# Kernel optimization log

Hardware: AMD Instinct MI355X
Metric: run time of the kernel (lower is better)

## Reference

```python
import jax, jax.numpy as jnp
import numpy as np

N_EMBD = 1024
N_HEAD = 16
HEAD_DIM = N_EMBD // N_HEAD
HIDDEN = int(2 * N_EMBD * 4 / 3)  # 2730, SwiGLU sizing from source
EPS = 1e-5


def setup_inputs() -> dict:
    key = jax.random.key(0)
    ks = jax.random.split(key, 16)
    def lin(k, fan_in, fan_out):
        bound = 1.0 / np.sqrt(fan_in)
        return jax.random.uniform(k, (fan_in, fan_out), jnp.float32, -bound, bound)
    return {
        "x": jax.random.normal(ks[0], (2, 2048, N_EMBD), jnp.float32),
        "ln1_g": jnp.ones((N_EMBD,), jnp.float32),
        "ln1_b": jnp.zeros((N_EMBD,), jnp.float32),
        "qkv_w": lin(ks[1], N_EMBD, 3 * N_EMBD),
        "qkv_b": jnp.zeros((3 * N_EMBD,), jnp.float32),
        "proj_w": lin(ks[2], N_EMBD, N_EMBD),
        "proj_b": jnp.zeros((N_EMBD,), jnp.float32),
        "ln2_g": jnp.ones((N_EMBD,), jnp.float32),
        "ln2_b": jnp.zeros((N_EMBD,), jnp.float32),
        "gate_w": lin(ks[3], N_EMBD, HIDDEN),
        "gate_b": jnp.zeros((HIDDEN,), jnp.float32),
        "up_w": lin(ks[4], N_EMBD, HIDDEN),
        "up_b": jnp.zeros((HIDDEN,), jnp.float32),
        "down_w": lin(ks[5], HIDDEN, N_EMBD),
        "down_b": jnp.zeros((N_EMBD,), jnp.float32),
    }


def _layernorm(x, g, b):
    mu = jnp.mean(x, axis=-1, keepdims=True)
    var = jnp.mean(jnp.square(x - mu), axis=-1, keepdims=True)
    return (x - mu) * jax.lax.rsqrt(var + EPS) * g + b


def _alibi_slopes(n_heads):
    i = jnp.arange(1, n_heads + 1, dtype=jnp.float32)
    return 1.0 / jnp.power(2.0, 8.0 * i / n_heads)  # [H]


def reference(x, ln1_g, ln1_b, qkv_w, qkv_b, proj_w, proj_b,
              ln2_g, ln2_b, gate_w, gate_b, up_w, up_b, down_w, down_b):
    B, T, C = x.shape
    residual = x
    h = _layernorm(x, ln1_g, ln1_b)
    qkv = h @ qkv_w + qkv_b  # [B,T,3C]
    q, k, v = jnp.split(qkv, 3, axis=-1)
    q = q.reshape(B, T, N_HEAD, HEAD_DIM).transpose(0, 2, 1, 3)
    k = k.reshape(B, T, N_HEAD, HEAD_DIM).transpose(0, 2, 1, 3)
    v = v.reshape(B, T, N_HEAD, HEAD_DIM).transpose(0, 2, 1, 3)
    scale = 1.0 / np.sqrt(HEAD_DIM)
    attn = jnp.einsum('bhqd,bhkd->bhqk', q, k) * scale
    # ALiBi: slope * |q_pos - k_pos| (abs distance, as in source)
    pos = jnp.arange(T)
    dist = jnp.abs(pos[None, :] - pos[:, None]).astype(jnp.float32)  # [T,T]
    slopes = _alibi_slopes(N_HEAD)  # [H]
    attn = attn + slopes[None, :, None, None] * dist[None, None, :, :]
    causal = pos[:, None] >= pos[None, :]  # tril mask
    attn = jnp.where(causal[None, None], attn, -jnp.inf)
    attn = jax.nn.softmax(attn, axis=-1)
    out = jnp.einsum('bhqk,bhkd->bhqd', attn, v)
    out = out.transpose(0, 2, 1, 3).reshape(B, T, C)
    out = out @ proj_w + proj_b
    x = residual + out
    residual = x
    h = _layernorm(x, ln2_g, ln2_b)
    gate = h @ gate_w + gate_b
    up = h @ up_w + up_b
    ff = (gate * jax.nn.sigmoid(gate) * up) @ down_w + down_b
    return residual + ff
```

## Files before the change

### kernel.cpp

```cpp
#include <hip/hip_runtime.h>
#include <cstdint>
#include <cstddef>

#define T_SEQ   2048
#define BATCH   2
#define NEMBD   1024
#define NHEAD   16
#define HDIM    64
#define HIDDEN  2730
#define HIDDENP 2816
#define MROWS   4096

typedef __bf16 bf16x8 __attribute__((ext_vector_type(8)));
typedef __bf16 bf16x4 __attribute__((ext_vector_type(4)));
typedef float  f32x4  __attribute__((ext_vector_type(4)));

__device__ __forceinline__ void gl2lds16(const void* g, void* l) {
    __builtin_amdgcn_global_load_lds((const __attribute__((address_space(1))) void*)g,
                                     (__attribute__((address_space(3))) void*)l, 16, 0, 0);
}

__global__ __launch_bounds__(256) void conv_trans(const float* __restrict__ W,
                                                  __bf16* __restrict__ Wt,
                                                  int K, int N, int Kp)
{
    __shared__ float tile[32][33];
    const int n0 = blockIdx.x * 32, k0 = blockIdx.y * 32;
    const int tx = threadIdx.x, ty = threadIdx.y;
#pragma unroll
    for (int i = ty; i < 32; i += 8) {
        int k = k0 + i, n = n0 + tx;
        tile[i][tx] = (k < K && n < N) ? W[(size_t)k * N + n] : 0.f;
    }
    __syncthreads();
#pragma unroll
    for (int i = ty; i < 32; i += 8) {
        int n = n0 + i, k = k0 + tx;
        Wt[(size_t)n * Kp + k] = (__bf16)tile[tx][i];
    }
}

__global__ __launch_bounds__(256) void ln_kernel(const float* __restrict__ x,
                                                 const float* __restrict__ g,
                                                 const float* __restrict__ b,
                                                 __bf16* __restrict__ out)
{
    const int row = blockIdx.x;
    const int t   = threadIdx.x;
    const float4 v = ((const float4*)(x + (size_t)row * NEMBD))[t];
    float s  = v.x + v.y + v.z + v.w;
    float sq = v.x * v.x + v.y * v.y + v.z * v.z + v.w * v.w;
#pragma unroll
    for (int d = 1; d < 64; d <<= 1) { s += __shfl_xor(s, d); sq += __shfl_xor(sq, d); }
    __shared__ float ssh[4], sqsh[4];
    const int w = t >> 6;
    if ((t & 63) == 0) { ssh[w] = s; sqsh[w] = sq; }
    __syncthreads();
    s  = ssh[0] + ssh[1] + ssh[2] + ssh[3];
    sq = sqsh[0] + sqsh[1] + sqsh[2] + sqsh[3];
    const float mean = s * (1.f / NEMBD);
    const float var  = sq * (1.f / NEMBD) - mean * mean;
    const float rstd = rsqrtf(var + 1e-5f);
    const float4 gg = ((const float4*)g)[t];
    const float4 bb = ((const float4*)b)[t];
    bf16x4 o;
    o[0] = (__bf16)((v.x - mean) * rstd * gg.x + bb.x);
    o[1] = (__bf16)((v.y - mean) * rstd * gg.y + bb.y);
    o[2] = (__bf16)((v.z - mean) * rstd * gg.z + bb.z);
    o[3] = (__bf16)((v.w - mean) * rstd * gg.w + bb.w);
    *(bf16x4*)&out[(size_t)row * NEMBD + t * 4] = o;
}

template <int MODE>
__global__ __launch_bounds__(256) void gemm_bt(const __bf16* __restrict__ A,
                                               const __bf16* __restrict__ Bt,
                                               const float* __restrict__ bias, int Nreal,
                                               const float* __restrict__ res,
                                               const __bf16* __restrict__ gbuf,
                                               void* __restrict__ outp,
                                               void* __restrict__ outp2,
                                               int Kp, int N)
{
    __shared__ alignas(16) __bf16 Ash[128 * 32];
    __shared__ alignas(16) __bf16 Bsh[128 * 32];
    const int tid  = threadIdx.x;
    const int w    = tid >> 6, l = tid & 63;
    const int ln   = l & 15, quad = l >> 4;
    const int wm   = w >> 1, wn = w & 1;
    const long m0  = (long)blockIdx.y * 128;
    const long n0  = (long)blockIdx.x * 128;
    f32x4 acc[4][4] = {};
    const __bf16* Ab = A + m0 * Kp;
    const __bf16* Bb = Bt + n0 * Kp;
    const int arow = l >> 2, acol = (l & 3) * 8;

    for (int k0 = 0; k0 < Kp; k0 += 32) {
#pragma unroll
        for (int it = 0; it < 2; ++it) {
            const int c = w * 2 + it;
            gl2lds16(Ab + (long)(c * 16 + arow) * Kp + k0 + acol, Ash + c * 512);
            gl2lds16(Bb + (long)(c * 16 + arow) * Kp + k0 + acol, Bsh + c * 512);
        }
        __syncthreads();
        bf16x8 af[4], bfr[4];
#pragma unroll
        for (int i = 0; i < 4; ++i) {
            af[i]  = *(const bf16x8*)&Ash[(wm * 64 + i * 16 + ln) * 32 + quad * 8];
            bfr[i] = *(const bf16x8*)&Bsh[(wn * 64 + i * 16 + ln) * 32 + quad * 8];
        }
#pragma unroll
        for (int tm = 0; tm < 4; ++tm)
#pragma unroll
            for (int tn = 0; tn < 4; ++tn)
                acc[tm][tn] = __builtin_amdgcn_mfma_f32_16x16x32_bf16(af[tm], bfr[tn], acc[tm][tn], 0, 0, 0);
        __syncthreads();
    }

    if (MODE == 3 && n0 >= 2048) {
        __bf16* vt = (__bf16*)outp2;
        const long bbq    = m0 >> 11;
        const long t0base = (m0 & 2047) + wm * 64;
#pragma unroll
        for (int tm = 0; tm < 4; ++tm)
#pragma unroll
            for (int tn = 0; tn < 4; ++tn) {
                const long col = n0 + wn * 64 + tn * 16 + ln;
                const float bv = bias[col];
                bf16x4 pv;
#pragma unroll
                for (int r = 0; r < 4; ++r) pv[r] = (__bf16)(acc[tm][tn][r] + bv);
                const long tt = t0base + tm * 16 + quad * 4;
                *(bf16x4*)&vt[(bbq * 1024 + (col - 2048)) * 2048 + tt] = pv;
            }
        return;
    }

#pragma unroll
    for (int tm = 0; tm < 4; ++tm)
#pragma unroll
        for (int tn = 0; tn < 4; ++tn) {
            const long col = n0 + wn * 64 + tn * 16 + ln;
            const float bv = (col < Nreal) ? bias[col] : 0.f;
#pragma unroll
            for (int r = 0; r < 4; ++r) {
                const long row = m0 + wm * 64 + tm * 16 + quad * 4 + r;
                float v = acc[tm][tn][r] + bv;
                if (MODE == 0) {
                    ((__bf16*)outp)[row * N + col] = (__bf16)v;
                } else if (MODE == 1) {
                    ((float*)outp)[row * N + col] = v + res[row * N + col];
                } else if (MODE == 2) {
                    const float gg = (float)gbuf[row * N + col];
                    const float sg = gg / (1.f + __expf(-gg));
                    ((__bf16*)outp)[row * N + col] = (__bf16)(sg * v);
                } else {
                    ((__bf16*)outp)[row * 2048 + col] = (__bf16)v;
                }
            }
        }
}

__global__ __launch_bounds__(256) void attn_kernel(const __bf16* __restrict__ qk,
                                                   const __bf16* __restrict__ vT,
                                                   __bf16* __restrict__ out)
{
    __shared__ alignas(16) __bf16 Ksh[64 * 64];
    __shared__ alignas(16) __bf16 Vtsh[64 * 64];
    __shared__ alignas(16) __bf16 Psh[4][32 * 64];

    const int tid = threadIdx.x;
    const int w   = tid >> 6, l = tid & 63;
    const int ln  = l & 15, quad = l >> 4;
    const int bh  = blockIdx.x;
    const int qt  = 15 - blockIdx.y;
    const int bb  = bh >> 4, hh = bh & 15;
    const long bT = (long)bb * T_SEQ;
    const int q0b = qt * 128;
    const int q0w = q0b + w * 32;
    const float slope = exp2f(-0.5f * (float)(hh + 1));

    bf16x8 qf[2][2];
#pragma unroll
    for (int q2 = 0; q2 < 2; ++q2) {
        const __bf16* qp = qk + (bT + q0w + q2 * 16 + ln) * 2048 + hh * 64 + quad * 8;
        qf[q2][0] = *(const bf16x8*)qp;
        qf[q2][1] = *(const bf16x8*)(qp + 32);
    }

    f32x4 o[2][4] = {};
    float mrun[2][4], lrun[2][4];
#pragma unroll
    for (int q2 = 0; q2 < 2; ++q2)
#pragma unroll
        for (int r = 0; r < 4; ++r) { mrun[q2][r] = -1e30f; lrun[q2][r] = 0.f; }

    const int sw = ln & 7;
    const int kmax = q0b + 128;
    for (int k0 = 0; k0 < kmax; k0 += 64) {
        __syncthreads();
#pragma unroll
        for (int jj = 0; jj < 2; ++jj) {
            const int j   = w * 2 + jj;
            const int row = j * 8 + (l >> 3);
            const int seg = (l & 7) ^ (row & 7);
            gl2lds16(qk + (bT + k0 + row) * 2048 + 1024 + hh * 64 + seg * 8,
                     Ksh + j * 8 * 64);
            gl2lds16(vT + ((long)(bb * 1024 + hh * 64 + row)) * 2048 + k0 + seg * 8,
                     Vtsh + j * 8 * 64);
        }
        __syncthreads();

        if (k0 <= q0w + 31) {
            const bool act0 = (k0 <= q0w + 15);
            f32x4 s0[4], s1[4];
#pragma unroll
            for (int kt = 0; kt < 4; ++kt) { s0[kt] = (f32x4){0,0,0,0}; s1[kt] = (f32x4){0,0,0,0}; }
#pragma unroll
            for (int kt = 0; kt < 4; ++kt)
#pragma unroll
                for (int kh = 0; kh < 2; ++kh) {
                    const bf16x8 kf = *(const bf16x8*)&Ksh[(kt * 16 + ln) * 64 + (((kh * 4 + quad) ^ sw) << 3)];
                    if (act0) s0[kt] = __builtin_amdgcn_mfma_f32_16x16x32_bf16(qf[0][kh], kf, s0[kt], 0, 0, 0);
                    s1[kt] = __builtin_amdgcn_mfma_f32_16x16x32_bf16(qf[1][kh], kf, s1[kt], 0, 0, 0);
                }
            float alpha[2][4];
#pragma unroll
            for (int q2 = 0; q2 < 2; ++q2) {
                if (q2 == 0 && !act0) continue;
                f32x4* s = (q2 == 0) ? s0 : s1;
                const int qbase = q0w + q2 * 16;
                float rmax[4];
#pragma unroll
                for (int r = 0; r < 4; ++r) {
                    const int qrow = qbase + quad * 4 + r;
                    float mv = -1e30f;
#pragma unroll
                    for (int kt = 0; kt < 4; ++kt) {
                        const int kc = k0 + kt * 16 + ln;
                        float v = s[kt][r] * 0.125f + slope * (float)(qrow - kc);
                        v = (kc <= qrow) ? v : -1e30f;
                        s[kt][r] = v;
                        mv = fmaxf(mv, v);
                    }
                    rmax[r] = mv;
                }
#pragma unroll
                for (int d = 1; d < 16; d <<= 1)
#pragma unroll
                    for (int r = 0; r < 4; ++r) rmax[r] = fmaxf(rmax[r], __shfl_xor(rmax[r], d));
                float rsum[4];
#pragma unroll
                for (int r = 0; r < 4; ++r) {
                    const float mnew = fmaxf(mrun[q2][r], rmax[r]);
                    alpha[q2][r] = __expf(mrun[q2][r] - mnew);
                    mrun[q2][r]  = mnew;
                    float t = 0.f;
#pragma unroll
                    for (int kt = 0; kt < 4; ++kt) {
                        const float e = __expf(s[kt][r] - mnew);
                        s[kt][r] = e;
                        t += e;
                    }
                    rsum[r] = t;
                }
#pragma unroll
                for (int d = 1; d < 16; d <<= 1)
#pragma unroll
                    for (int r = 0; r < 4; ++r) rsum[r] += __shfl_xor(rsum[r], d);
#pragma unroll
                for (int r = 0; r < 4; ++r) lrun[q2][r] = lrun[q2][r] * alpha[q2][r] + rsum[r];
#pragma unroll
                for (int kt = 0; kt < 4; ++kt)
#pragma unroll
                    for (int r = 0; r < 4; ++r) {
                        const int q = q2 * 16 + quad * 4 + r;
                        Psh[w][q * 64 + (((kt * 2 + (ln >> 3)) ^ (q & 7)) << 3) + (ln & 7)] = (__bf16)s[kt][r];
                    }
#pragma unroll
                for (int dt = 0; dt < 4; ++dt)
#pragma unroll
                    for (int r = 0; r < 4; ++r) o[q2][dt][r] *= alpha[q2][r];
            }
            asm volatile("s_waitcnt lgkmcnt(0)" ::: "memory");
#pragma unroll
            for (int kh2 = 0; kh2 < 2; ++kh2) {
                bf16x8 pf0, pf1;
                if (act0) pf0 = *(const bf16x8*)&Psh[w][(ln)*64 + (((kh2 * 4 + quad) ^ sw) << 3)];
                pf1 = *(const bf16x8*)&Psh[w][(16 + ln) * 64 + (((kh2 * 4 + quad) ^ sw) << 3)];
#pragma unroll
                for (int dt = 0; dt < 4; ++dt) {
                    const bf16x8 vf = *(const bf16x8*)&Vtsh[(dt * 16 + ln) * 64 + (((kh2 * 4 + quad) ^ sw) << 3)];
                    if (act0) o[0][dt] = __builtin_amdgcn_mfma_f32_16x16x32_bf16(pf0, vf, o[0][dt], 0, 0, 0);
                    o[1][dt] = __builtin_amdgcn_mfma_f32_16x16x32_bf16(pf1, vf, o[1][dt], 0, 0, 0);
                }
            }
        }
    }
#pragma unroll
    for (int q2 = 0; q2 < 2; ++q2)
#pragma unroll
        for (int dt = 0; dt < 4; ++dt)
#pragma unroll
            for (int r = 0; r < 4; ++r) {
                const long row = bT + q0w + q2 * 16 + quad * 4 + r;
                out[row * NEMBD + hh * 64 + dt * 16 + ln] = (__bf16)(o[q2][dt][r] / lrun[q2][r]);
            }
}

extern "C" void kernel_launch(void* const* d_in, const int* in_sizes, int n_in,
                              void* d_out, int out_size, void* d_ws, size_t ws_size,
                              hipStream_t stream)
{
    const float* x      = (const float*)d_in[0];
    const float* ln1_g  = (const float*)d_in[1];
    const float* ln1_b  = (const float*)d_in[2];
    const float* qkv_w  = (const float*)d_in[3];
    const float* qkv_b  = (const float*)d_in[4];
    const float* proj_w = (const float*)d_in[5];
    const float* proj_b = (const float*)d_in[6];
    const float* ln2_g  = (const float*)d_in[7];
    const float* ln2_b  = (const float*)d_in[8];
    const float* gate_w = (const float*)d_in[9];
    const float* gate_b = (const float*)d_in[10];
    const float* up_w   = (const float*)d_in[11];
    const float* up_b   = (const float*)d_in[12];
    const float* down_w = (const float*)d_in[13];
    const float* down_b = (const float*)d_in[14];
    float* out = (float*)d_out;
    char*  ws  = (char*)d_ws;

    const size_t OFF_WQKV  = 0;
    const size_t OFF_WPROJ = 6291456;
    const size_t OFF_WGATE = 8388608;
    const size_t OFF_WUP   = 14155776;
    const size_t OFF_WDOWN = 19922944;
    const size_t OFF_H     = 25690112;
    const size_t OFF_QK    = 34078720;
    const size_t OFF_VT    = 50855936;
    const size_t OFF_G     = OFF_QK;
    const size_t OFF_ATTN  = 59244544;
    const size_t OFF_FF    = 67633152;
    const size_t NEED      = 90701824;
    if (ws_size < NEED) return;

    __bf16* wqkv  = (__bf16*)(ws + OFF_WQKV);
    __bf16* wproj = (__bf16*)(ws + OFF_WPROJ);
    __bf16* wgate = (__bf16*)(ws + OFF_WGATE);
    __bf16* wup   = (__bf16*)(ws + OFF_WUP);
    __bf16* wdown = (__bf16*)(ws + OFF_WDOWN);
    __bf16* hbuf  = (__bf16*)(ws + OFF_H);
    __bf16* qkb   = (__bf16*)(ws + OFF_QK);
    __bf16* vtb   = (__bf16*)(ws + OFF_VT);
    __bf16* gbuf  = (__bf16*)(ws + OFF_G);
    __bf16* attnb = (__bf16*)(ws + OFF_ATTN);
    __bf16* ffbuf = (__bf16*)(ws + OFF_FF);

    const dim3 tb(32, 8);
    conv_trans<<<dim3(96, 32), tb, 0, stream>>>(qkv_w,  wqkv,  1024, 3072, 1024);
    conv_trans<<<dim3(32, 32), tb, 0, stream>>>(proj_w, wproj, 1024, 1024, 1024);
    conv_trans<<<dim3(88, 32), tb, 0, stream>>>(gate_w, wgate, 1024, HIDDEN, 1024);
    conv_trans<<<dim3(88, 32), tb, 0, stream>>>(up_w,   wup,   1024, HIDDEN, 1024);
    conv_trans<<<dim3(32, 88), tb, 0, stream>>>(down_w, wdown, HIDDEN, 1024, HIDDENP);

    ln_kernel<<<MROWS, 256, 0, stream>>>(x, ln1_g, ln1_b, hbuf);
    gemm_bt<3><<<dim3(24, 32), 256, 0, stream>>>(hbuf, wqkv, qkv_b, 3072, nullptr, nullptr, qkb, vtb, 1024, 3072);
    attn_kernel<<<dim3(32, 16), 256, 0, stream>>>(qkb, vtb, attnb);
    gemm_bt<1><<<dim3(8, 32), 256, 0, stream>>>(attnb, wproj, proj_b, 1024, x, nullptr, out, nullptr, 1024, 1024);
    ln_kernel<<<MROWS, 256, 0, stream>>>(out, ln2_g, ln2_b, hbuf);
    gemm_bt<0><<<dim3(22, 32), 256, 0, stream>>>(hbuf, wgate, gate_b, HIDDEN, nullptr, nullptr, gbuf, nullptr, 1024, HIDDENP);
    gemm_bt<2><<<dim3(22, 32), 256, 0, stream>>>(hbuf, wup, up_b, HIDDEN, nullptr, gbuf, ffbuf, nullptr, 1024, HIDDENP);
    gemm_bt<1><<<dim3(8, 32), 256, 0, stream>>>(ffbuf, wdown, down_b, 1024, out, nullptr, out, nullptr, HIDDENP, 1024);
}
```

Measured before the change: 499.5 us.

## Double-buffer attention K/V loads, shrink query tiles, add half-height residual GEMM

The attention kernel now gives each block 64 query rows (16 per wave) instead of 128, which doubles the grid. It double-buffers the K/V tiles in LDS so the next chunk's global-to-LDS load overlaps the current chunk's compute, and it skips the causal mask on chunks that lie fully below the diagonal. The residual-add GEMMs (proj and down) move to a new 64x128 tile kernel with a 512-block grid, which should fill the CUs better for N=1024. The costs are more redundant K/V reads across query tiles, two barriers per chunk, and a simpler GEMM with no software pipelining.

```diff
diff --git a/kernel.cpp b/kernel.cpp
--- a/kernel.cpp
+++ b/kernel.cpp
@@ -147,8 +147,6 @@
                 float v = acc[tm][tn][r] + bv;
                 if (MODE == 0) {
                     ((__bf16*)outp)[row * N + col] = (__bf16)v;
-                } else if (MODE == 1) {
-                    ((float*)outp)[row * N + col] = v + res[row * N + col];
                 } else if (MODE == 2) {
                     const float gg = (float)gbuf[row * N + col];
                     const float sg = gg / (1.f + __expf(-gg));
@@ -160,151 +158,211 @@
         }
 }
 
-__global__ __launch_bounds__(256) void attn_kernel(const __bf16* __restrict__ qk,
-                                                   const __bf16* __restrict__ vT,
-                                                   __bf16* __restrict__ out)
-{
-    __shared__ alignas(16) __bf16 Ksh[64 * 64];
-    __shared__ alignas(16) __bf16 Vtsh[64 * 64];
-    __shared__ alignas(16) __bf16 Psh[4][32 * 64];
+__global__ __launch_bounds__(256) void gemm_bt_h(const __bf16* __restrict__ A,
+                                                 const __bf16* __restrict__ Bt,
+                                                 const float* __restrict__ bias,
+                                                 const float* __restrict__ res,
+                                                 float* __restrict__ outp, int Kp, int N)
+{
+    __shared__ alignas(16) __bf16 Ash[64 * 32];
+    __shared__ alignas(16) __bf16 Bsh[128 * 32];
+    const int tid  = threadIdx.x;
+    const int w    = tid >> 6, l = tid & 63;
+    const int ln   = l & 15, quad = l >> 4;
+    const int wm   = w >> 1, wn = w & 1;
+    const long m0  = (long)blockIdx.y * 64;
+    const long n0  = (long)blockIdx.x * 128;
+    f32x4 acc[2][4] = {};
+    const __bf16* Ab = A + m0 * Kp;
+    const __bf16* Bb = Bt + n0 * Kp;
+    const int arow = l >> 2, acol = (l & 3) * 8;
+
+    for (int k0 = 0; k0 < Kp; k0 += 32) {
+        gl2lds16(Ab + (long)(w * 16 + arow) * Kp + k0 + acol, Ash + w * 512);
+#pragma unroll
+        for (int it = 0; it < 2; ++it) {
+            const int c = w * 2 + it;
+            gl2lds16(Bb + (long)(c * 16 + arow) * Kp + k0 + acol, Bsh + c * 512);
+        }
+        __syncthreads();
+        bf16x8 af[2], bfr[4];
+#pragma unroll
+        for (int i = 0; i < 2; ++i)
+            af[i] = *(const bf16x8*)&Ash[(wm * 32 + i * 16 + ln) * 32 + quad * 8];
+#pragma unroll
+        for (int i = 0; i < 4; ++i)
+            bfr[i] = *(const bf16x8*)&Bsh[(wn * 64 + i * 16 + ln) * 32 + quad * 8];
+#pragma unroll
+        for (int tm = 0; tm < 2; ++tm)
+#pragma unroll
+            for (int tn = 0; tn < 4; ++tn)
+                acc[tm][tn] = __builtin_amdgcn_mfma_f32_16x16x32_bf16(af[tm], bfr[tn], acc[tm][tn], 0, 0, 0);
+        __syncthreads();
+    }
+
+#pragma unroll
+    for (int tm = 0; tm < 2; ++tm)
+#pragma unroll
+        for (int tn = 0; tn < 4; ++tn) {
+            const long col = n0 + wn * 64 + tn * 16 + ln;
+            const float bv = bias[col];
+#pragma unroll
+            for (int r = 0; r < 4; ++r) {
+                const long row = m0 + wm * 32 + tm * 16 + quad * 4 + r;
+                outp[row * N + col] = acc[tm][tn][r] + bv + res[row * N + col];
+            }
+        }
+}
+
+__device__ __forceinline__ void attn_stage(const __bf16* __restrict__ qk,
+                                           const __bf16* __restrict__ vT,
+                                           __bf16* Kd, __bf16* Vd,
+                                           long bT, int bb, int hh, int k0, int w, int l)
+{
+#pragma unroll
+    for (int jj = 0; jj < 2; ++jj) {
+        const int j   = w * 2 + jj;
+        const int row = j * 8 + (l >> 3);
+        const int seg = (l & 7) ^ (row & 7);
+        gl2lds16(qk + (bT + k0 + row) * 2048 + 1024 + hh * 64 + seg * 8, Kd + j * 512);
+        gl2lds16(vT + ((long)(bb * 1024 + hh * 64 + row)) * 2048 + k0 + seg * 8, Vd + j * 512);
+    }
+}
+
+__global__ __launch_bounds__(256, 4) void attn_kernel(const __bf16* __restrict__ qk,
+                                                      const __bf16* __restrict__ vT,
+                                                      __bf16* __restrict__ out)
+{
+    __shared__ alignas(16) __bf16 Ksh[2][64 * 64];
+    __shared__ alignas(16) __bf16 Vtsh[2][64 * 64];
+    __shared__ alignas(16) __bf16 Psh[4][16 * 64];
 
     const int tid = threadIdx.x;
     const int w   = tid >> 6, l = tid & 63;
     const int ln  = l & 15, quad = l >> 4;
     const int bh  = blockIdx.x;
-    const int qt  = 15 - blockIdx.y;
+    const int qt  = 31 - blockIdx.y;
     const int bb  = bh >> 4, hh = bh & 15;
     const long bT = (long)bb * T_SEQ;
-    const int q0b = qt * 128;
-    const int q0w = q0b + w * 32;
+    const int q0b = qt * 64;
+    const int q0w = q0b + w * 16;
     const float slope = exp2f(-0.5f * (float)(hh + 1));
 
-    bf16x8 qf[2][2];
-#pragma unroll
-    for (int q2 = 0; q2 < 2; ++q2) {
-        const __bf16* qp = qk + (bT + q0w + q2 * 16 + ln) * 2048 + hh * 64 + quad * 8;
-        qf[q2][0] = *(const bf16x8*)qp;
-        qf[q2][1] = *(const bf16x8*)(qp + 32);
-    }
-
-    f32x4 o[2][4] = {};
-    float mrun[2][4], lrun[2][4];
-#pragma unroll
-    for (int q2 = 0; q2 < 2; ++q2)
-#pragma unroll
-        for (int r = 0; r < 4; ++r) { mrun[q2][r] = -1e30f; lrun[q2][r] = 0.f; }
-
-    const int sw = ln & 7;
-    const int kmax = q0b + 128;
-    for (int k0 = 0; k0 < kmax; k0 += 64) {
-        __syncthreads();
-#pragma unroll
-        for (int jj = 0; jj < 2; ++jj) {
-            const int j   = w * 2 + jj;
-            const int row = j * 8 + (l >> 3);
-            const int seg = (l & 7) ^ (row & 7);
-            gl2lds16(qk + (bT + k0 + row) * 2048 + 1024 + hh * 64 + seg * 8,
-                     Ksh + j * 8 * 64);
-            gl2lds16(vT + ((long)(bb * 1024 + hh * 64 + row)) * 2048 + k0 + seg * 8,
-                     Vtsh + j * 8 * 64);
-        }
-        __syncthreads();
-
-        if (k0 <= q0w + 31) {
-            const bool act0 = (k0 <= q0w + 15);
-            f32x4 s0[4], s1[4];
-#pragma unroll
-            for (int kt = 0; kt < 4; ++kt) { s0[kt] = (f32x4){0,0,0,0}; s1[kt] = (f32x4){0,0,0,0}; }
-#pragma unroll
-            for (int kt = 0; kt < 4; ++kt)
-#pragma unroll
-                for (int kh = 0; kh < 2; ++kh) {
-                    const bf16x8 kf = *(const bf16x8*)&Ksh[(kt * 16 + ln) * 64 + (((kh * 4 + quad) ^ sw) << 3)];
-                    if (act0) s0[kt] = __builtin_amdgcn_mfma_f32_16x16x32_bf16(qf[0][kh], kf, s0[kt], 0, 0, 0);
-                    s1[kt] = __builtin_amdgcn_mfma_f32_16x16x32_bf16(qf[1][kh], kf, s1[kt], 0, 0, 0);
-                }
-            float alpha[2][4];
-#pragma unroll
-            for (int q2 = 0; q2 < 2; ++q2) {
-                if (q2 == 0 && !act0) continue;
-                f32x4* s = (q2 == 0) ? s0 : s1;
-                const int qbase = q0w + q2 * 16;
-                float rmax[4];
-#pragma unroll
-                for (int r = 0; r < 4; ++r) {
-                    const int qrow = qbase + quad * 4 + r;
-                    float mv = -1e30f;
-#pragma unroll
-                    for (int kt = 0; kt < 4; ++kt) {
-                        const int kc = k0 + kt * 16 + ln;
-                        float v = s[kt][r] * 0.125f + slope * (float)(qrow - kc);
-                        v = (kc <= qrow) ? v : -1e30f;
-                        s[kt][r] = v;
-                        mv = fmaxf(mv, v);
-                    }
-                    rmax[r] = mv;
-                }
-#pragma unroll
-                for (int d = 1; d < 16; d <<= 1)
-#pragma unroll
-                    for (int r = 0; r < 4; ++r) rmax[r] = fmaxf(rmax[r], __shfl_xor(rmax[r], d));
-                float rsum[4];
-#pragma unroll
-                for (int r = 0; r < 4; ++r) {
-                    const float mnew = fmaxf(mrun[q2][r], rmax[r]);
-                    alpha[q2][r] = __expf(mrun[q2][r] - mnew);
-                    mrun[q2][r]  = mnew;
-                    float t = 0.f;
-#pragma unroll
-                    for (int kt = 0; kt < 4; ++kt) {
-                        const float e = __expf(s[kt][r] - mnew);
-                        s[kt][r] = e;
-                        t += e;
-                    }
-                    rsum[r] = t;
-                }
-#pragma unroll
-                for (int d = 1; d < 16; d <<= 1)
-#pragma unroll
-                    for (int r = 0; r < 4; ++r) rsum[r] += __shfl_xor(rsum[r], d);
-#pragma unroll
-                for (int r = 0; r < 4; ++r) lrun[q2][r] = lrun[q2][r] * alpha[q2][r] + rsum[r];
-#pragma unroll
-                for (int kt = 0; kt < 4; ++kt)
-#pragma unroll
-                    for (int r = 0; r < 4; ++r) {
-                        const int q = q2 * 16 + quad * 4 + r;
-                        Psh[w][q * 64 + (((kt * 2 + (ln >> 3)) ^ (q & 7)) << 3) + (ln & 7)] = (__bf16)s[kt][r];
-                    }
-#pragma unroll
-                for (int dt = 0; dt < 4; ++dt)
-#pragma unroll
-                    for (int r = 0; r < 4; ++r) o[q2][dt][r] *= alpha[q2][r];
-            }
-            asm volatile("s_waitcnt lgkmcnt(0)" ::: "memory");
-#pragma unroll
-            for (int kh2 = 0; kh2 < 2; ++kh2) {
-                bf16x8 pf0, pf1;
-                if (act0) pf0 = *(const bf16x8*)&Psh[w][(ln)*64 + (((kh2 * 4 + quad) ^ sw) << 3)];
-                pf1 = *(const bf16x8*)&Psh[w][(16 + ln) * 64 + (((kh2 * 4 + quad) ^ sw) << 3)];
-#pragma unroll
-                for (int dt = 0; dt < 4; ++dt) {
-                    const bf16x8 vf = *(const bf16x8*)&Vtsh[(dt * 16 + ln) * 64 + (((kh2 * 4 + quad) ^ sw) << 3)];
-                    if (act0) o[0][dt] = __builtin_amdgcn_mfma_f32_16x16x32_bf16(pf0, vf, o[0][dt], 0, 0, 0);
-                    o[1][dt] = __builtin_amdgcn_mfma_f32_16x16x32_bf16(pf1, vf, o[1][dt], 0, 0, 0);
-                }
-            }
-        }
-    }
-#pragma unroll
-    for (int q2 = 0; q2 < 2; ++q2)
+    bf16x8 qf0, qf1;
+    {
+        const __bf16* qp = qk + (bT + q0w + ln) * 2048 + hh * 64 + quad * 8;
+        qf0 = *(const bf16x8*)qp;
+        qf1 = *(const bf16x8*)(qp + 32);
+    }
+
+    f32x4 o[4] = {};
+    float mrun[4], lrun[4];
+#pragma unroll
+    for (int r = 0; r < 4; ++r) { mrun[r] = -1e30f; lrun[r] = 0.f; }
+
+    const int sw  = ln & 7;
+    const int nch = qt + 1;
+
+    attn_stage(qk, vT, Ksh[0], Vtsh[0], bT, bb, hh, 0, w, l);
+
+    for (int i = 0; i < nch; ++i) {
+        const int k0  = i * 64;
+        const int cur = i & 1;
+        if (i + 1 < nch) {
+            attn_stage(qk, vT, Ksh[cur ^ 1], Vtsh[cur ^ 1], bT, bb, hh, k0 + 64, w, l);
+            asm volatile("s_waitcnt vmcnt(4)" ::: "memory");
+        } else {
+            asm volatile("s_waitcnt vmcnt(0)" ::: "memory");
+        }
+        __builtin_amdgcn_s_barrier();
+
+        f32x4 s[4];
+#pragma unroll
+        for (int kt = 0; kt < 4; ++kt) s[kt] = (f32x4){0.f, 0.f, 0.f, 0.f};
+#pragma unroll
+        for (int kt = 0; kt < 4; ++kt) {
+            bf16x8 kf;
+            kf = *(const bf16x8*)&Ksh[cur][(kt * 16 + ln) * 64 + (((0 * 4 + quad) ^ sw) << 3)];
+            s[kt] = __builtin_amdgcn_mfma_f32_16x16x32_bf16(qf0, kf, s[kt], 0, 0, 0);
+            kf = *(const bf16x8*)&Ksh[cur][(kt * 16 + ln) * 64 + (((1 * 4 + quad) ^ sw) << 3)];
+            s[kt] = __builtin_amdgcn_mfma_f32_16x16x32_bf16(qf1, kf, s[kt], 0, 0, 0);
+        }
+
+        float tk[4];
+#pragma unroll
+        for (int kt = 0; kt < 4; ++kt) tk[kt] = -slope * (float)(k0 + kt * 16 + ln);
+        const bool full = (k0 + 64 <= q0w);
+        float rmax[4];
+#pragma unroll
+        for (int r = 0; r < 4; ++r) {
+            const int qrow = q0w + quad * 4 + r;
+            float mv = -1e30f;
+#pragma unroll
+            for (int kt = 0; kt < 4; ++kt) {
+                float v = fmaf(s[kt][r], 0.125f, tk[kt]);
+                if (!full) v = (k0 + kt * 16 + ln <= qrow) ? v : -1e30f;
+                s[kt][r] = v;
+                mv = fmaxf(mv, v);
+            }
+            rmax[r] = mv;
+        }
+#pragma unroll
+        for (int d = 1; d < 16; d <<= 1)
+#pragma unroll
+            for (int r = 0; r < 4; ++r) rmax[r] = fmaxf(rmax[r], __shfl_xor(rmax[r], d));
+        float alpha[4], rsum[4];
+#pragma unroll
+        for (int r = 0; r < 4; ++r) {
+            const float mnew = fmaxf(mrun[r], rmax[r]);
+            alpha[r] = __expf(mrun[r] - mnew);
+            mrun[r]  = mnew;
+            float t = 0.f;
+#pragma unroll
+            for (int kt = 0; kt < 4; ++kt) {
+                const float e = __expf(s[kt][r] - mnew);
+                s[kt][r] = e;
+                t += e;
+            }
+            rsum[r] = t;
+        }
+#pragma unroll
+        for (int d = 1; d < 16; d <<= 1)
+#pragma unroll
+            for (int r = 0; r < 4; ++r) rsum[r] += __shfl_xor(rsum[r], d);
+#pragma unroll
+        for (int r = 0; r < 4; ++r) lrun[r] = lrun[r] * alpha[r] + rsum[r];
+
+#pragma unroll
+        for (int kt = 0; kt < 4; ++kt)
+#pragma unroll
+            for (int r = 0; r < 4; ++r) {
+                const int q = quad * 4 + r;
+                Psh[w][q * 64 + (((kt * 2 + (ln >> 3)) ^ (q & 7)) << 3) + (ln & 7)] = (__bf16)s[kt][r];
+            }
+        asm volatile("s_waitcnt lgkmcnt(0)" ::: "memory");
 #pragma unroll
         for (int dt = 0; dt < 4; ++dt)
 #pragma unroll
-            for (int r = 0; r < 4; ++r) {
-                const long row = bT + q0w + q2 * 16 + quad * 4 + r;
-                out[row * NEMBD + hh * 64 + dt * 16 + ln] = (__bf16)(o[q2][dt][r] / lrun[q2][r]);
-            }
+            for (int r = 0; r < 4; ++r) o[dt][r] *= alpha[r];
+#pragma unroll
+        for (int kh2 = 0; kh2 < 2; ++kh2) {
+            const bf16x8 pfr = *(const bf16x8*)&Psh[w][ln * 64 + (((kh2 * 4 + quad) ^ sw) << 3)];
+#pragma unroll
+            for (int dt = 0; dt < 4; ++dt) {
+                const bf16x8 vf = *(const bf16x8*)&Vtsh[cur][(dt * 16 + ln) * 64 + (((kh2 * 4 + quad) ^ sw) << 3)];
+                o[dt] = __builtin_amdgcn_mfma_f32_16x16x32_bf16(pfr, vf, o[dt], 0, 0, 0);
+            }
+        }
+        __builtin_amdgcn_s_barrier();
+    }
+
+#pragma unroll
+    for (int dt = 0; dt < 4; ++dt)
+#pragma unroll
+        for (int r = 0; r < 4; ++r) {
+            const long row = bT + q0w + quad * 4 + r;
+            out[row * NEMBD + hh * 64 + dt * 16 + ln] = (__bf16)(o[dt][r] / lrun[r]);
+        }
 }
 
 extern "C" void kernel_launch(void* const* d_in, const int* in_sizes, int n_in,
@@ -364,10 +422,10 @@
 
     ln_kernel<<<MROWS, 256, 0, stream>>>(x, ln1_g, ln1_b, hbuf);
     gemm_bt<3><<<dim3(24, 32), 256, 0, stream>>>(hbuf, wqkv, qkv_b, 3072, nullptr, nullptr, qkb, vtb, 1024, 3072);
-    attn_kernel<<<dim3(32, 16), 256, 0, stream>>>(qkb, vtb, attnb);
-    gemm_bt<1><<<dim3(8, 32), 256, 0, stream>>>(attnb, wproj, proj_b, 1024, x, nullptr, out, nullptr, 1024, 1024);
+    attn_kernel<<<dim3(32, 32), 256, 0, stream>>>(qkb, vtb, attnb);
+    gemm_bt_h<<<dim3(8, 64), 256, 0, stream>>>(attnb, wproj, proj_b, x, out, 1024, 1024);
     ln_kernel<<<MROWS, 256, 0, stream>>>(out, ln2_g, ln2_b, hbuf);
     gemm_bt<0><<<dim3(22, 32), 256, 0, stream>>>(hbuf, wgate, gate_b, HIDDEN, nullptr, nullptr, gbuf, nullptr, 1024, HIDDENP);
     gemm_bt<2><<<dim3(22, 32), 256, 0, stream>>>(hbuf, wup, up_b, HIDDEN, nullptr, gbuf, ffbuf, nullptr, 1024, HIDDENP);
-    gemm_bt<1><<<dim3(8, 32), 256, 0, stream>>>(ffbuf, wdown, down_b, 1024, out, nullptr, out, nullptr, HIDDENP, 1024);
-}
+    gemm_bt_h<<<dim3(8, 64), 256, 0, stream>>>(ffbuf, wdown, down_b, out, out, HIDDENP, 1024);
+}
```

New measurement: 433.9 us. 13.1% less time.
